# Kernel tuning notes

Measured on AMD Instinct MI355X. Metric: run time of the kernel, lower is better.

## Reference

```python
import jax, jax.numpy as jnp
import numpy as np

DEPTH = 2          # number of transformer blocks
DIM = 1280         # hidden_size
NHEADS = 16
HDIM = DIM // NHEADS  # 80
FF = 5120          # intermediate_size
S = 8192           # total ragged tokens
NSEG = 8           # number of image segments
EPS = 1e-6
GRID = 32          # per-image patch grid side (32*32*8 = 8192)


def _rotate_half(x):
    h = x.shape[-1] // 2
    return jnp.concatenate([-x[..., h:], x[..., :h]], axis=-1)


def _layernorm(x, g, b):
    mu = jnp.mean(x, axis=-1, keepdims=True)
    var = jnp.mean(jnp.square(x - mu), axis=-1, keepdims=True)
    return (x - mu) * jax.lax.rsqrt(var + EPS) * g + b


def setup_inputs() -> dict:
    key = jax.random.key(0)
    ks = jax.random.split(key, 16)
    std = 0.02
    hidden_states = jax.random.normal(ks[0], (S, DIM), jnp.float32)
    cu_seqlens = jnp.arange(NSEG + 1, dtype=jnp.int32) * (S // NSEG)
    # 2D rotary: per-axis freq table of size head_dim//4, concat row+col -> head_dim//2,
    # duplicated (cat(freqs, freqs)) -> head_dim, then cos/sin.
    rot_dim = HDIM // 2
    inv_freq = 1.0 / (10000.0 ** (jnp.arange(0, rot_dim, 2, dtype=jnp.float32) / rot_dim))  # [HDIM//4]
    tok = jnp.arange(S)
    rows = ((tok % (GRID * GRID)) // GRID).astype(jnp.float32)
    cols = (tok % GRID).astype(jnp.float32)
    freqs = jnp.concatenate([rows[:, None] * inv_freq[None, :], cols[:, None] * inv_freq[None, :]], axis=-1)  # [S, HDIM//2]
    emb = jnp.concatenate([freqs, freqs], axis=-1)  # [S, HDIM]
    cos = jnp.cos(emb)
    sin = jnp.sin(emb)
    def rnd(k, shape):
        return jax.random.normal(k, shape, jnp.float32) * std
    params = {
        'ln1_g': jnp.ones((DEPTH, DIM), jnp.float32), 'ln1_b': jnp.zeros((DEPTH, DIM), jnp.float32),
        'ln2_g': jnp.ones((DEPTH, DIM), jnp.float32), 'ln2_b': jnp.zeros((DEPTH, DIM), jnp.float32),
        'qkv_w': rnd(ks[1], (DEPTH, 3 * DIM, DIM)), 'qkv_b': jnp.zeros((DEPTH, 3 * DIM), jnp.float32),
        'proj_w': rnd(ks[2], (DEPTH, DIM, DIM)), 'proj_b': jnp.zeros((DEPTH, DIM), jnp.float32),
        'fc1_w': rnd(ks[3], (DEPTH, FF, DIM)), 'fc1_b': jnp.zeros((DEPTH, FF), jnp.float32),
        'fc2_w': rnd(ks[4], (DEPTH, DIM, FF)), 'fc2_b': jnp.zeros((DEPTH, DIM), jnp.float32),
    }
    return dict(hidden_states=hidden_states, cu_seqlens=cu_seqlens, cos=cos, sin=sin, **params)


def reference(hidden_states, cu_seqlens, cos, sin,
              ln1_g, ln1_b, ln2_g, ln2_b,
              qkv_w, qkv_b, proj_w, proj_b,
              fc1_w, fc1_b, fc2_w, fc2_b):
    seq = hidden_states.shape[0]
    # cu_seqlens is a static (int) input; derive the block-diagonal segmentation.
    seg = np.diff(np.asarray(jax.device_get(cu_seqlens)))
    L = int(seg[0])
    assert (seg == L).all(), 'reference assumes equal-length segments'
    n = len(seg)
    scale = HDIM ** -0.5
    c = cos[:, None, :]  # broadcast over heads, like cos.unsqueeze(1)
    s_ = sin[:, None, :]
    x = hidden_states
    for i in range(DEPTH):
        # --- attention ---
        h = _layernorm(x, ln1_g[i], ln1_b[i])
        qkv = (h @ qkv_w[i].T + qkv_b[i]).reshape(seq, 3, NHEADS, HDIM)
        q, k, v = qkv[:, 0], qkv[:, 1], qkv[:, 2]
        q = q * c + _rotate_half(q) * s_
        k = k * c + _rotate_half(k) * s_
        qs = q.reshape(n, L, NHEADS, HDIM)
        ks_ = k.reshape(n, L, NHEADS, HDIM)
        vs = v.reshape(n, L, NHEADS, HDIM)
        # block-diagonal (per-segment) attention, fp32 softmax
        attn = jnp.einsum('nlhd,nkhd->nhlk', qs, ks_) * scale
        p = jax.nn.softmax(attn, axis=-1)
        o = jnp.einsum('nhlk,nkhd->nlhd', p, vs).reshape(seq, DIM)
        x = x + (o @ proj_w[i].T + proj_b[i])
        # --- mlp (gelu tanh approx) ---
        h2 = _layernorm(x, ln2_g[i], ln2_b[i])
        x = x + (jax.nn.gelu(h2 @ fc1_w[i].T + fc1_b[i], approximate=True) @ fc2_w[i].T + fc2_b[i])
    return x
```

## Files before the change

### kernel.cpp

```cpp
#include <hip/hip_runtime.h>
#include <hip/hip_bf16.h>

typedef __attribute__((ext_vector_type(8))) short bf16x8;
typedef __attribute__((ext_vector_type(4))) float f32x4;
typedef __attribute__((ext_vector_type(8))) unsigned short u16x8;

__device__ __forceinline__ void gload_lds16(const void* g, void* l) {
  __builtin_amdgcn_global_load_lds(
      (const __attribute__((address_space(1))) unsigned int*)g,
      (__attribute__((address_space(3))) unsigned int*)l, 16, 0, 0);
}

__device__ __forceinline__ unsigned short f2bfu(float f) {
  __hip_bfloat16 h = __float2bfloat16(f);
  return __builtin_bit_cast(unsigned short, h);
}

__global__ __launch_bounds__(256) void copy_f32(const float* __restrict__ in,
                                                float* __restrict__ out, int n) {
  for (int i = blockIdx.x * 256 + threadIdx.x; i < n; i += gridDim.x * 256)
    out[i] = in[i];
}

__global__ __launch_bounds__(256) void w2bf(const float* __restrict__ in,
                                            __hip_bfloat16* __restrict__ out, int n) {
  for (int i = blockIdx.x * 256 + threadIdx.x; i < n; i += gridDim.x * 256)
    out[i] = __float2bfloat16(in[i]);
}

__global__ __launch_bounds__(256) void ln_kernel(const float* __restrict__ x,
                                                 const float* __restrict__ g,
                                                 const float* __restrict__ b,
                                                 __hip_bfloat16* __restrict__ h) {
  const int row = blockIdx.x;
  const int tid = threadIdx.x;
  const float* xr = x + (size_t)row * 1280;
  float v[5];
  float s = 0.f;
#pragma unroll
  for (int i = 0; i < 5; i++) { v[i] = xr[tid + i * 256]; s += v[i]; }
#pragma unroll
  for (int off = 32; off >= 1; off >>= 1) s += __shfl_xor(s, off);
  __shared__ float red[8];
  const int w = tid >> 6, lane = tid & 63;
  if (lane == 0) red[w] = s;
  __syncthreads();
  const float mu = (red[0] + red[1] + red[2] + red[3]) * (1.f / 1280.f);
  float q = 0.f;
#pragma unroll
  for (int i = 0; i < 5; i++) { float d = v[i] - mu; q += d * d; }
#pragma unroll
  for (int off = 32; off >= 1; off >>= 1) q += __shfl_xor(q, off);
  if (lane == 0) red[4 + w] = q;
  __syncthreads();
  const float var = (red[4] + red[5] + red[6] + red[7]) * (1.f / 1280.f);
  const float rstd = rsqrtf(var + 1e-6f);
#pragma unroll
  for (int i = 0; i < 5; i++) {
    int c = tid + i * 256;
    h[(size_t)row * 1280 + c] = __float2bfloat16((v[i] - mu) * rstd * g[c] + b[c]);
  }
}

__global__ __launch_bounds__(256) void rope_kernel(__hip_bfloat16* __restrict__ qkv,
                                                   const float* __restrict__ cs,
                                                   const float* __restrict__ sn) {
  const int TOT = 8192 * 2 * 16 * 40;
  for (int idx = blockIdx.x * 256 + threadIdx.x; idx < TOT; idx += gridDim.x * 256) {
    int d = idx % 40;
    int t = idx / 40;
    int head = t & 15;
    int t2 = t >> 4;
    int part = t2 & 1;
    int s = t2 >> 1;
    size_t base = ((size_t)s * 3 + part) * 1280 + head * 80;
    float e0 = __bfloat162float(qkv[base + d]);
    float e1 = __bfloat162float(qkv[base + d + 40]);
    float c0 = cs[s * 80 + d];
    float s0 = sn[s * 80 + d];
    float c1 = cs[s * 80 + d + 40];
    float s1 = sn[s * 80 + d + 40];
    qkv[base + d]      = __float2bfloat16(e0 * c0 - e1 * s0);
    qkv[base + d + 40] = __float2bfloat16(e1 * c1 + e0 * s1);
  }
}

__global__ __launch_bounds__(256) void vtrans_kernel(const __hip_bfloat16* __restrict__ qkv,
                                                     __hip_bfloat16* __restrict__ vt) {
  const int idx = blockIdx.x * 256 + threadIdx.x;
  const int s = idx & 8191;
  const int dc = idx >> 13;
  const unsigned short* src = (const unsigned short*)qkv + ((size_t)s * 3 + 2) * 1280 + dc * 8;
  u16x8 v = *(const u16x8*)src;
  unsigned short* dst = (unsigned short*)vt + (size_t)dc * 8 * 8192 + s;
#pragma unroll
  for (int j = 0; j < 8; j++) dst[(size_t)j * 8192] = v[j];
}

#define VMCNT4 asm volatile("s_waitcnt vmcnt(4)" ::: "memory")

#define MFMAQ(MH, NH)                                                                      \
  __builtin_amdgcn_s_barrier();                                                            \
  __builtin_amdgcn_s_setprio(1);                                                           \
  _Pragma("unroll") for (int kk = 0; kk < 2; kk++)                                         \
  _Pragma("unroll") for (int mm = 0; mm < 4; mm++)                                         \
  _Pragma("unroll") for (int nn = 0; nn < 2; nn++)                                         \
    acc[(MH) * 4 + mm][(NH) * 2 + nn] = __builtin_amdgcn_mfma_f32_16x16x32_bf16(           \
        af[mm][kk], bq[NH][nn][kk], acc[(MH) * 4 + mm][(NH) * 2 + nn], 0, 0, 0);           \
  __builtin_amdgcn_s_setprio(0);

template <int EPI>
__global__ __launch_bounds__(512, 2) void gemm256(const __hip_bfloat16* __restrict__ A,
                                                  const __hip_bfloat16* __restrict__ B,
                                                  const float* __restrict__ bias,
                                                  __hip_bfloat16* __restrict__ C,
                                                  float* __restrict__ X,
                                                  int M, int N, int K) {
  __shared__ __align__(16) char lds[131072];
  const int tid = threadIdx.x, lane = tid & 63, w = tid >> 6;
  const int wr = w >> 2, wc = w & 3;
  const int lm = lane & 15, hi = lane >> 4;

  const int nby = M >> 8, nbx = N >> 8;
  const int xcd = blockIdx.x & 7;
  const int local = blockIdx.x >> 3;
  const int by = xcd * (nby >> 3) + local / nbx;
  const int bx = local % nbx;
  const long mBase = (long)by << 8, nBase = (long)bx << 8;

  f32x4 acc[8][4];
#pragma unroll
  for (int m = 0; m < 8; m++)
#pragma unroll
    for (int n = 0; n < 4; n++) acc[m][n] = (f32x4){0.f, 0.f, 0.f, 0.f};

  const int r0 = (w << 3) + (lane >> 3);
  const int slotT = (lane & 7) ^ (lane >> 3);
  const unsigned short* Ag = (const unsigned short*)A;
  const unsigned short* Bg = (const unsigned short*)B;
  const size_t aB = (size_t)(mBase + r0) * K + slotT * 8;
  const size_t bB = (size_t)(nBase + r0) * K + slotT * 8;
  const int wdst = w << 10;

  auto STAGE = [&](int tile, int half, int isB) {
    char* dst = lds + ((tile & 1) << 16) + (isB << 15) + (half << 14) + wdst;
    const unsigned short* src =
        (isB ? Bg + bB : Ag + aB) + (size_t)(half << 7) * (size_t)K + ((size_t)tile << 6);
    gload_lds16(src, dst);
    gload_lds16(src + ((size_t)K << 6), dst + 8192);
  };

  const int rowA = (wr * 64 + lm) * 128;
  const int rowB = (wc * 32 + lm) * 128 + 32768;
  const int key = lm & 7;
  int sw_s[2];
#pragma unroll
  for (int kk = 0; kk < 2; kk++) sw_s[kk] = (((kk << 2) | hi) ^ key) << 4;

  const int nt = K >> 6;

  STAGE(0, 0, 0); STAGE(0, 0, 1); STAGE(0, 1, 1); STAGE(0, 1, 0);
  STAGE(1, 0, 0); STAGE(1, 0, 1);
  VMCNT4;
  __builtin_amdgcn_s_barrier();

  for (int t = 0; t < nt; ++t) {
    const int bufOff = (t & 1) << 16;
    const bool s1 = t + 1 < nt, s2 = t + 2 < nt;
    bf16x8 af[4][2], bq[2][2][2];
#pragma unroll
    for (int mm = 0; mm < 4; mm++)
#pragma unroll
      for (int kk = 0; kk < 2; kk++)
        af[mm][kk] = *(const bf16x8*)(lds + bufOff + rowA + mm * 2048 + sw_s[kk]);
#pragma unroll
    for (int nh = 0; nh < 2; nh++)
#pragma unroll
      for (int nn = 0; nn < 2; nn++)
#pragma unroll
        for (int kk = 0; kk < 2; kk++)
          bq[nh][nn][kk] =
              *(const bf16x8*)(lds + bufOff + nh * 16384 + rowB + nn * 2048 + sw_s[kk]);
    if (s1) STAGE(t + 1, 1, 1);
    MFMAQ(0, 0);
    __builtin_amdgcn_s_barrier();
    if (s1) STAGE(t + 1, 1, 0);
    MFMAQ(0, 1);
    __builtin_amdgcn_s_barrier();
#pragma unroll
    for (int mm = 0; mm < 4; mm++)
#pragma unroll
      for (int kk = 0; kk < 2; kk++)
        af[mm][kk] = *(const bf16x8*)(lds + bufOff + 16384 + rowA + mm * 2048 + sw_s[kk]);
    if (s2) STAGE(t + 2, 0, 0);
    MFMAQ(1, 0);
    __builtin_amdgcn_s_barrier();
    if (s2) STAGE(t + 2, 0, 1);
    MFMAQ(1, 1);
    VMCNT4;
    __builtin_amdgcn_s_barrier();
  }

#pragma unroll
  for (int n = 0; n < 4; n++) {
    const int col = (int)nBase + (n >> 1) * 128 + wc * 32 + (n & 1) * 16 + lm;
    const float bv = bias[col];
#pragma unroll
    for (int m = 0; m < 8; m++) {
      const int er = (int)mBase + (m >> 2) * 128 + wr * 64 + (m & 3) * 16 + hi * 4;
#pragma unroll
      for (int j = 0; j < 4; j++) {
        float v = acc[m][n][j] + bv;
        size_t off = (size_t)(er + j) * N + col;
        if constexpr (EPI == 0) {
          C[off] = __float2bfloat16(v);
        } else if constexpr (EPI == 1) {
          float u = v + 0.044715f * v * v * v;
          float E = exp2f(2.30220818f * u);
          float t2 = 1.f - 2.f / (E + 1.f);
          C[off] = __float2bfloat16(0.5f * v * (1.f + t2));
        } else {
          X[off] += v;
        }
      }
    }
  }
}

__global__ __launch_bounds__(512, 4) void attn_kernel(const __hip_bfloat16* __restrict__ qkv,
                                                      const __hip_bfloat16* __restrict__ vtg,
                                                      __hip_bfloat16* __restrict__ o) {
  __shared__ __align__(16) unsigned short Ks[128 * 96];
  __shared__ __align__(16) unsigned short Vt[80 * 136];
  __shared__ __align__(16) unsigned short Ps[8][16 * 68];
  const int tid = threadIdx.x, lane = tid & 63, w = tid >> 6;
  const int lm = lane & 15, hi = lane >> 4;
  const int qt = blockIdx.x, head = blockIdx.y, seg = blockIdx.z;
  const int s0 = seg * 1024;
  const int qrow0 = s0 + qt * 128;
  const unsigned short* qg = (const unsigned short*)qkv;
  const unsigned short* vg = (const unsigned short*)vtg + (size_t)head * 80 * 8192;

  for (int idx = tid; idx < 2048; idx += 512) {
    int r = idx >> 4, c = 80 + (idx & 15);
    Ks[r * 96 + c] = 0;
  }

  bf16x8 aq[3];
  {
    const unsigned short* qrow = qg + (size_t)(qrow0 + w * 16 + lm) * 3840 + head * 80;
#pragma unroll
    for (int kk = 0; kk < 3; kk++) aq[kk] = *(const bf16x8*)(qrow + kk * 32 + hi * 8);
  }

  auto loadKV = [&](int kt, u16x8* kr, u16x8* vr) {
#pragma unroll
    for (int it = 0; it < 3; it++) {
      int c = tid + it * 512;
      if (c < 1280) {
        int r = c / 10, c8 = c % 10;
        kr[it] = *(const u16x8*)(qg + ((size_t)(s0 + kt * 128 + r) * 3 + 1) * 1280 +
                                 head * 80 + c8 * 8);
        int d = c >> 4, sc = c & 15;
        vr[it] = *(const u16x8*)(vg + (size_t)d * 8192 + s0 + kt * 128 + sc * 8);
      }
    }
  };
  auto writeKV = [&](u16x8* kr, u16x8* vr) {
#pragma unroll
    for (int it = 0; it < 3; it++) {
      int c = tid + it * 512;
      if (c < 1280) {
        int r = c / 10, c8 = c % 10;
        *(u16x8*)&Ks[r * 96 + c8 * 8] = kr[it];
        int d = c >> 4, sc = c & 15;
        *(u16x8*)&Vt[d * 136 + sc * 8] = vr[it];
      }
    }
  };

  {
    u16x8 kr[3], vr[3];
    loadKV(0, kr, vr);
    writeKV(kr, vr);
  }
  __syncthreads();

  float m_s[4] = {-1e30f, -1e30f, -1e30f, -1e30f};
  float l_s[4] = {0.f, 0.f, 0.f, 0.f};
  f32x4 accO[5];
#pragma unroll
  for (int nf = 0; nf < 5; nf++) accO[nf] = (f32x4){0.f, 0.f, 0.f, 0.f};

  const float SM = 0.11180339887498949f * 1.4426950408889634f;

  for (int kt = 0; kt < 8; kt++) {
    u16x8 krn[3], vrn[3];
    if (kt + 1 < 8) loadKV(kt + 1, krn, vrn);

    f32x4 sf[8];
#pragma unroll
    for (int n = 0; n < 8; n++) sf[n] = (f32x4){0.f, 0.f, 0.f, 0.f};
#pragma unroll
    for (int kk = 0; kk < 3; kk++) {
#pragma unroll
      for (int n = 0; n < 8; n++) {
        bf16x8 bk = *(const bf16x8*)(&Ks[(n * 16 + lm) * 96 + kk * 32 + hi * 8]);
        sf[n] = __builtin_amdgcn_mfma_f32_16x16x32_bf16(aq[kk], bk, sf[n], 0, 0, 0);
      }
    }

    float alpha[4];
#pragma unroll
    for (int j = 0; j < 4; j++) {
      float v = sf[0][j];
#pragma unroll
      for (int n = 1; n < 8; n++) v = fmaxf(v, sf[n][j]);
#pragma unroll
      for (int off = 1; off < 16; off <<= 1) v = fmaxf(v, __shfl_xor(v, off));
      float mn = fmaxf(m_s[j], v);
      alpha[j] = exp2f((m_s[j] - mn) * SM);
      m_s[j] = mn;
    }
    float rsum[4] = {0.f, 0.f, 0.f, 0.f};
#pragma unroll
    for (int n = 0; n < 8; n++)
#pragma unroll
      for (int j = 0; j < 4; j++) {
        float p = exp2f((sf[n][j] - m_s[j]) * SM);
        sf[n][j] = p;
        rsum[j] += p;
      }
#pragma unroll
    for (int j = 0; j < 4; j++) {
#pragma unroll
      for (int off = 1; off < 16; off <<= 1) rsum[j] += __shfl_xor(rsum[j], off);
      l_s[j] = l_s[j] * alpha[j] + rsum[j];
    }
#pragma unroll
    for (int nf = 0; nf < 5; nf++)
#pragma unroll
      for (int j = 0; j < 4; j++) accO[nf][j] *= alpha[j];

#pragma unroll
    for (int h = 0; h < 2; h++) {
#pragma unroll
      for (int n = 0; n < 4; n++)
#pragma unroll
        for (int j = 0; j < 4; j++)
          Ps[w][(hi * 4 + j) * 68 + n * 16 + lm] = f2bfu(sf[h * 4 + n][j]);
#pragma unroll
      for (int kk = 0; kk < 2; kk++) {
        bf16x8 pa = *(const bf16x8*)(&Ps[w][lm * 68 + kk * 32 + hi * 8]);
#pragma unroll
        for (int nf = 0; nf < 5; nf++) {
          bf16x8 bv =
              *(const bf16x8*)(&Vt[(nf * 16 + lm) * 136 + h * 64 + kk * 32 + hi * 8]);
          accO[nf] = __builtin_amdgcn_mfma_f32_16x16x32_bf16(pa, bv, accO[nf], 0, 0, 0);
        }
      }
    }

    __syncthreads();
    if (kt + 1 < 8) writeKV(krn, vrn);
    __syncthreads();
  }

#pragma unroll
  for (int nf = 0; nf < 5; nf++) {
    int d = nf * 16 + lm;
#pragma unroll
    for (int j = 0; j < 4; j++) {
      int r = qrow0 + w * 16 + hi * 4 + j;
      o[(size_t)r * 1280 + head * 80 + d] = __float2bfloat16(accO[nf][j] / l_s[j]);
    }
  }
}

extern "C" void kernel_launch(void* const* d_in, const int* in_sizes, int n_in,
                              void* d_out, int out_size, void* d_ws, size_t ws_size,
                              hipStream_t stream) {
  (void)in_sizes; (void)n_in; (void)out_size; (void)ws_size;
  const float* hidden = (const float*)d_in[0];
  const float* cs   = (const float*)d_in[2];
  const float* sn   = (const float*)d_in[3];
  const float* ln1g = (const float*)d_in[4];
  const float* ln1b = (const float*)d_in[5];
  const float* ln2g = (const float*)d_in[6];
  const float* ln2b = (const float*)d_in[7];
  const float* qkvw = (const float*)d_in[8];
  const float* qkvb = (const float*)d_in[9];
  const float* pw   = (const float*)d_in[10];
  const float* pb   = (const float*)d_in[11];
  const float* f1w  = (const float*)d_in[12];
  const float* f1b  = (const float*)d_in[13];
  const float* f2w  = (const float*)d_in[14];
  const float* f2b  = (const float*)d_in[15];

  float* x = (float*)d_out;

  char* ws = (char*)d_ws;
  __hip_bfloat16* h    = (__hip_bfloat16*)ws;
  __hip_bfloat16* vt   = (__hip_bfloat16*)ws;
  __hip_bfloat16* qkv  = (__hip_bfloat16*)(ws + 20971520);
  __hip_bfloat16* o    = (__hip_bfloat16*)(ws + 83886080);
  __hip_bfloat16* ffh  = (__hip_bfloat16*)(ws + 20971520);
  __hip_bfloat16* wbuf = (__hip_bfloat16*)(ws + 104857600);

  const int NTOK = 8192 * 1280;
  copy_f32<<<2048, 256, 0, stream>>>(hidden, x, NTOK);
  for (int i = 0; i < 2; i++) {
    ln_kernel<<<8192, 256, 0, stream>>>(x, ln1g + i * 1280, ln1b + i * 1280, h);

    w2bf<<<2048, 256, 0, stream>>>(qkvw + (size_t)i * 3840 * 1280, wbuf, 3840 * 1280);
    gemm256<0><<<480, 512, 0, stream>>>(h, wbuf, qkvb + i * 3840, qkv, nullptr,
                                        8192, 3840, 1280);
    vtrans_kernel<<<5120, 256, 0, stream>>>(qkv, vt);
    rope_kernel<<<4096, 256, 0, stream>>>(qkv, cs, sn);
    attn_kernel<<<dim3(8, 16, 8), 512, 0, stream>>>(qkv, vt, o);

    w2bf<<<2048, 256, 0, stream>>>(pw + (size_t)i * 1280 * 1280, wbuf, 1280 * 1280);
    gemm256<2><<<160, 512, 0, stream>>>(o, wbuf, pb + i * 1280, nullptr, x,
                                        8192, 1280, 1280);

    ln_kernel<<<8192, 256, 0, stream>>>(x, ln2g + i * 1280, ln2b + i * 1280, h);

    w2bf<<<2048, 256, 0, stream>>>(f1w + (size_t)i * 5120 * 1280, wbuf, 5120 * 1280);
    gemm256<1><<<640, 512, 0, stream>>>(h, wbuf, f1b + i * 5120, ffh, nullptr,
                                        8192, 5120, 1280);

    w2bf<<<2048, 256, 0, stream>>>(f2w + (size_t)i * 1280 * 5120, wbuf, 1280 * 5120);
    gemm256<2><<<160, 512, 0, stream>>>(ffh, wbuf, f2b + i * 1280, nullptr, x,
                                        8192, 1280, 5120);
  }
}
```

Baseline: 1.367 ms.

## Restructure GEMM K-loop phases, stage epilogue through LDS, add lazy softmax rescale

The GEMM main loop goes from four MFMA quarters with interleaved staging to two halves, each issuing both stage loads before a barrier. A vmcnt(0) wait is added at the second-to-last iteration. The epilogue now writes accumulators plus bias into per-wave LDS scratch and reads them back as rows, so global stores and the residual read-modify-write use 4-wide vectors instead of scalar strided writes. The attention kernel only rescales the running max and accumulators when some row's max grows past a threshold, and raises wave priority around its MFMA blocks. Together these aim to cut barrier count, uncoalesced epilogue traffic and per-tile rescale work, at the cost of less overlap between loads and MFMAs, extra LDS traffic in the epilogue, and a deferred-max softmax whose exponentials may exceed 1 before normalization.

Result: faster. 1.283 ms (-6.2%).

```diff
diff --git a/kernel.cpp b/kernel.cpp
--- a/kernel.cpp
+++ b/kernel.cpp
@@ -4,6 +4,7 @@
 typedef __attribute__((ext_vector_type(8))) short bf16x8;
 typedef __attribute__((ext_vector_type(4))) float f32x4;
 typedef __attribute__((ext_vector_type(8))) unsigned short u16x8;
+typedef __attribute__((ext_vector_type(4))) unsigned short u16x4;
 
 __device__ __forceinline__ void gload_lds16(const void* g, void* l) {
   __builtin_amdgcn_global_load_lds(
@@ -98,16 +99,7 @@
 }
 
 #define VMCNT4 asm volatile("s_waitcnt vmcnt(4)" ::: "memory")
-
-#define MFMAQ(MH, NH)                                                                      \
-  __builtin_amdgcn_s_barrier();                                                            \
-  __builtin_amdgcn_s_setprio(1);                                                           \
-  _Pragma("unroll") for (int kk = 0; kk < 2; kk++)                                         \
-  _Pragma("unroll") for (int mm = 0; mm < 4; mm++)                                         \
-  _Pragma("unroll") for (int nn = 0; nn < 2; nn++)                                         \
-    acc[(MH) * 4 + mm][(NH) * 2 + nn] = __builtin_amdgcn_mfma_f32_16x16x32_bf16(           \
-        af[mm][kk], bq[NH][nn][kk], acc[(MH) * 4 + mm][(NH) * 2 + nn], 0, 0, 0);           \
-  __builtin_amdgcn_s_setprio(0);
+#define VMCNT0 asm volatile("s_waitcnt vmcnt(0)" ::: "memory")
 
 template <int EPI>
 __global__ __launch_bounds__(512, 2) void gemm256(const __hip_bfloat16* __restrict__ A,
@@ -181,50 +173,90 @@
         for (int kk = 0; kk < 2; kk++)
           bq[nh][nn][kk] =
               *(const bf16x8*)(lds + bufOff + nh * 16384 + rowB + nn * 2048 + sw_s[kk]);
-    if (s1) STAGE(t + 1, 1, 1);
-    MFMAQ(0, 0);
+    if (s1) { STAGE(t + 1, 1, 1); STAGE(t + 1, 1, 0); }
     __builtin_amdgcn_s_barrier();
-    if (s1) STAGE(t + 1, 1, 0);
-    MFMAQ(0, 1);
+    __builtin_amdgcn_s_setprio(1);
+#pragma unroll
+    for (int kk = 0; kk < 2; kk++)
+#pragma unroll
+      for (int mm = 0; mm < 4; mm++)
+#pragma unroll
+        for (int n = 0; n < 4; n++)
+          acc[mm][n] = __builtin_amdgcn_mfma_f32_16x16x32_bf16(
+              af[mm][kk], bq[n >> 1][n & 1][kk], acc[mm][n], 0, 0, 0);
+    __builtin_amdgcn_s_setprio(0);
     __builtin_amdgcn_s_barrier();
 #pragma unroll
     for (int mm = 0; mm < 4; mm++)
 #pragma unroll
       for (int kk = 0; kk < 2; kk++)
         af[mm][kk] = *(const bf16x8*)(lds + bufOff + 16384 + rowA + mm * 2048 + sw_s[kk]);
-    if (s2) STAGE(t + 2, 0, 0);
-    MFMAQ(1, 0);
+    if (s2) { STAGE(t + 2, 0, 0); STAGE(t + 2, 0, 1); }
     __builtin_amdgcn_s_barrier();
-    if (s2) STAGE(t + 2, 0, 1);
-    MFMAQ(1, 1);
-    VMCNT4;
+    __builtin_amdgcn_s_setprio(1);
+#pragma unroll
+    for (int kk = 0; kk < 2; kk++)
+#pragma unroll
+      for (int mm = 0; mm < 4; mm++)
+#pragma unroll
+        for (int n = 0; n < 4; n++)
+          acc[4 + mm][n] = __builtin_amdgcn_mfma_f32_16x16x32_bf16(
+              af[mm][kk], bq[n >> 1][n & 1][kk], acc[4 + mm][n], 0, 0, 0);
+    __builtin_amdgcn_s_setprio(0);
+    if (t == nt - 2) { VMCNT0; } else { VMCNT4; }
     __builtin_amdgcn_s_barrier();
   }
 
-#pragma unroll
-  for (int n = 0; n < 4; n++) {
-    const int col = (int)nBase + (n >> 1) * 128 + wc * 32 + (n & 1) * 16 + lm;
-    const float bv = bias[col];
-#pragma unroll
-    for (int m = 0; m < 8; m++) {
-      const int er = (int)mBase + (m >> 2) * 128 + wr * 64 + (m & 3) * 16 + hi * 4;
-#pragma unroll
-      for (int j = 0; j < 4; j++) {
-        float v = acc[m][n][j] + bv;
-        size_t off = (size_t)(er + j) * N + col;
+  float* eb = (float*)(lds + w * 9216);
+  float bvv[2][2];
+#pragma unroll
+  for (int nh = 0; nh < 2; nh++)
+#pragma unroll
+    for (int nn = 0; nn < 2; nn++)
+      bvv[nh][nn] = bias[nBase + nh * 128 + wc * 32 + nn * 16 + lm];
+
+#pragma unroll
+  for (int mh = 0; mh < 2; mh++)
+#pragma unroll
+    for (int nh = 0; nh < 2; nh++) {
+#pragma unroll
+      for (int mm = 0; mm < 4; mm++)
+#pragma unroll
+        for (int nn = 0; nn < 2; nn++)
+#pragma unroll
+          for (int j = 0; j < 4; j++)
+            eb[(mm * 16 + hi * 4 + j) * 36 + nn * 16 + lm] =
+                acc[mh * 4 + mm][nh * 2 + nn][j] + bvv[nh][nn];
+#pragma unroll
+      for (int rr = 0; rr < 8; rr++) {
+        const int r = rr * 8 + (lane >> 3);
+        const int c = (lane & 7) * 4;
+        f32x4 v = *(const f32x4*)&eb[r * 36 + c];
+        const int grow = (int)mBase + mh * 128 + wr * 64 + r;
+        const int gcol = (int)nBase + nh * 128 + wc * 32 + c;
+        const size_t off = (size_t)grow * N + gcol;
         if constexpr (EPI == 0) {
-          C[off] = __float2bfloat16(v);
+          u16x4 o4;
+#pragma unroll
+          for (int q = 0; q < 4; q++) o4[q] = f2bfu(v[q]);
+          *(u16x4*)((__hip_bfloat16*)C + off) = o4;
         } else if constexpr (EPI == 1) {
-          float u = v + 0.044715f * v * v * v;
-          float E = exp2f(2.30220818f * u);
-          float t2 = 1.f - 2.f / (E + 1.f);
-          C[off] = __float2bfloat16(0.5f * v * (1.f + t2));
+          u16x4 o4;
+#pragma unroll
+          for (int q = 0; q < 4; q++) {
+            float u = v[q] + 0.044715f * v[q] * v[q] * v[q];
+            float E = exp2f(2.30220818f * u);
+            float th = 1.f - 2.f / (E + 1.f);
+            o4[q] = f2bfu(0.5f * v[q] * (1.f + th));
+          }
+          *(u16x4*)((__hip_bfloat16*)C + off) = o4;
         } else {
-          X[off] += v;
+          f32x4 x = *(const f32x4*)&X[off];
+          x += v;
+          *(f32x4*)&X[off] = x;
         }
       }
     }
-  }
 }
 
 __global__ __launch_bounds__(512, 4) void attn_kernel(const __hip_bfloat16* __restrict__ qkv,
@@ -301,6 +333,7 @@
     f32x4 sf[8];
 #pragma unroll
     for (int n = 0; n < 8; n++) sf[n] = (f32x4){0.f, 0.f, 0.f, 0.f};
+    __builtin_amdgcn_s_setprio(1);
 #pragma unroll
     for (int kk = 0; kk < 3; kk++) {
 #pragma unroll
@@ -309,8 +342,10 @@
         sf[n] = __builtin_amdgcn_mfma_f32_16x16x32_bf16(aq[kk], bk, sf[n], 0, 0, 0);
       }
     }
-
-    float alpha[4];
+    __builtin_amdgcn_s_setprio(0);
+
+    float vmax[4];
+    float growth = -1e30f;
 #pragma unroll
     for (int j = 0; j < 4; j++) {
       float v = sf[0][j];
@@ -318,9 +353,19 @@
       for (int n = 1; n < 8; n++) v = fmaxf(v, sf[n][j]);
 #pragma unroll
       for (int off = 1; off < 16; off <<= 1) v = fmaxf(v, __shfl_xor(v, off));
-      float mn = fmaxf(m_s[j], v);
-      alpha[j] = exp2f((m_s[j] - mn) * SM);
-      m_s[j] = mn;
+      vmax[j] = v;
+      growth = fmaxf(growth, (v - m_s[j]) * SM);
+    }
+    if (__any(growth > 12.0f)) {
+#pragma unroll
+      for (int j = 0; j < 4; j++) {
+        float mn = fmaxf(m_s[j], vmax[j]);
+        float alpha = exp2f((m_s[j] - mn) * SM);
+        m_s[j] = mn;
+        l_s[j] *= alpha;
+#pragma unroll
+        for (int nf = 0; nf < 5; nf++) accO[nf][j] *= alpha;
+      }
     }
     float rsum[4] = {0.f, 0.f, 0.f, 0.f};
 #pragma unroll
@@ -335,12 +380,8 @@
     for (int j = 0; j < 4; j++) {
 #pragma unroll
       for (int off = 1; off < 16; off <<= 1) rsum[j] += __shfl_xor(rsum[j], off);
-      l_s[j] = l_s[j] * alpha[j] + rsum[j];
-    }
-#pragma unroll
-    for (int nf = 0; nf < 5; nf++)
-#pragma unroll
-      for (int j = 0; j < 4; j++) accO[nf][j] *= alpha[j];
+      l_s[j] += rsum[j];
+    }
 
 #pragma unroll
     for (int h = 0; h < 2; h++) {
@@ -349,6 +390,7 @@
 #pragma unroll
         for (int j = 0; j < 4; j++)
           Ps[w][(hi * 4 + j) * 68 + n * 16 + lm] = f2bfu(sf[h * 4 + n][j]);
+      __builtin_amdgcn_s_setprio(1);
 #pragma unroll
       for (int kk = 0; kk < 2; kk++) {
         bf16x8 pa = *(const bf16x8*)(&Ps[w][lm * 68 + kk * 32 + hi * 8]);
@@ -359,6 +401,7 @@
           accO[nf] = __builtin_amdgcn_mfma_f32_16x16x32_bf16(pa, bv, accO[nf], 0, 0, 0);
         }
       }
+      __builtin_amdgcn_s_setprio(0);
     }
 
     __syncthreads();
```
